# Kernel optimization log

Measured on AMD Instinct MI355X. Metric: run time of the kernel, lower is better.

## Reference

```python
import jax, jax.numpy as jnp
import numpy as np

HID = 16  # comparator hidden channels, Conv1(2,16) -> Conv1(16,1)


def setup_inputs() -> dict:
    key = jax.random.key(0)
    k0, k1, k2 = jax.random.split(key, 3)
    B, N = 32, 512
    x = jax.random.normal(k0, (B, 1, N), dtype=jnp.float32)
    # xavier_uniform for 1x1 convs, zero bias (as in PermNet.__init__)
    g1 = (6.0 / (2 + HID)) ** 0.5
    g2 = (6.0 / (HID + 1)) ** 0.5
    w1 = jax.random.uniform(k1, (HID, 2), jnp.float32, -g1, g1)
    b1 = jnp.zeros((HID,), jnp.float32)
    w2 = jax.random.uniform(k2, (1, HID), jnp.float32, -g2, g2)
    b2 = jnp.zeros((1,), jnp.float32)
    lr = jnp.ones((1,), jnp.float32)  # learned step size, used via abs()
    return {"x": x, "w1": w1, "b1": b1, "w2": w2, "b2": b2, "lr": lr,
            "steps": 8, "temp": 1}


def reference(x, w1, b1, w2, b2, lr, steps, temp):
    B, C, N = x.shape  # C == 1 (scalar set elements)
    temp = jnp.asarray(temp, x.dtype)

    # --- Comparator: pairwise 1x1-conv MLP over all (i, j) pairs ---
    xi = jnp.broadcast_to(x[:, 0, :, None], (B, N, N))  # element i
    xj = jnp.broadcast_to(x[:, 0, None, :], (B, N, N))  # element j
    pairs = jnp.stack([xi, xj], axis=1)                  # (B, 2, N, N)
    h = jax.nn.relu(jnp.einsum('oc,bcij->boij', w1, pairs)
                    + b1[None, :, None, None])           # (B, HID, N, N)
    c = (jnp.einsum('oc,bcij->boij', w2, h)
         + b2[None, :, None, None])[:, 0]                # (B, N, N)
    c = c - jnp.swapaxes(c, -1, -2)  # antisymmetric ordering cost C(i,j)=-C(j,i)

    # --- calculate_assignment: iterative differentiable permutation ---
    # a[b, i, k] = weight of element i being placed at position k
    lr_abs = jnp.abs(lr)[0]
    a0 = jnp.full((B, N, N), 1.0 / N, dtype=x.dtype)

    def step(a, _):
        csum = jnp.cumsum(a, axis=-1)      # sum_{l<=k} a[., j, l]
        total = csum[..., -1:]
        left = csum - a                     # sum_{l<k}
        right = total - csum                # sum_{l>k}
        m = right - left                    # (B, N, N)
        # d(total cost)/d a_{ik} = sum_j C_{ij} * (right_{jk} - left_{jk})
        grad = jnp.einsum('bij,bjk->bik', c, m)
        a_new = jax.nn.softmax((a - lr_abs * grad) / temp, axis=-1)
        return a_new, None

    a, _ = jax.lax.scan(step, a0, None, length=steps)

    # --- apply_assignment: permute elements into positions ---
    y = jnp.einsum('bci,bik->bck', x, a)  # (B, 1, N)
    return y, a
```

## Files before the change

### kernel.cpp

```cpp
#include <hip/hip_runtime.h>
#include <hip/hip_bf16.h>
#include <math.h>

#define B_   32
#define N_   512
#define HID_ 16

typedef __attribute__((ext_vector_type(8))) short bf16x8;
typedef __attribute__((ext_vector_type(4))) float f32x4;

union U8 { ushort u[8]; uint4 v; };
union U4 { ushort u[4]; uint2 v; };

__device__ __forceinline__ ushort f2bf(float f) {
    __hip_bfloat16 h = __float2bfloat16(f);
    return *reinterpret_cast<ushort*>(&h);
}
__device__ __forceinline__ float bf2f(ushort u) {
    return __uint_as_float(((unsigned int)u) << 16);
}

__device__ __forceinline__ void gload16(const void* g, void* l) {
    __builtin_amdgcn_global_load_lds(
        (const __attribute__((address_space(1))) unsigned int*)g,
        (__attribute__((address_space(3))) unsigned int*)l,
        16, 0, 0);
}

__device__ __forceinline__ int pidx(int r, int c) {
    return r * N_ + ((c + ((r >> 3) << 2)) & (N_ - 1));
}

__global__ __launch_bounds__(256)
void init_kernel(const float* __restrict__ x,
                 const float* __restrict__ w1,
                 const float* __restrict__ b1,
                 const float* __restrict__ w2,
                 ushort* __restrict__ cB,
                 float* __restrict__ v)
{
    __shared__ float sw1[2*HID_], sb1[HID_], sw2[HID_];
    __shared__ float red[4];
    int tid = threadIdx.x;
    if (tid < 2*HID_) sw1[tid] = w1[tid];
    if (tid < HID_)   { sb1[tid] = b1[tid]; sw2[tid] = w2[tid]; }
    __syncthreads();

    int rowg = blockIdx.x * 2 + (tid >> 7);
    int b    = rowg >> 9;
    int col  = (tid & 127) * 4;
    float xi = x[rowg];
    float4 xj = *(const float4*)&x[b*N_ + col];
    float xjv[4] = {xj.x, xj.y, xj.z, xj.w};

    float s1[4] = {}, s2[4] = {};
#pragma unroll
    for (int o = 0; o < HID_; ++o) {
        float wa = sw1[2*o], wb = sw1[2*o+1], bo = sb1[o], wo = sw2[o];
        float Ao = fmaf(wa, xi, bo);
        float Co = fmaf(wb, xi, bo);
#pragma unroll
        for (int e = 0; e < 4; ++e) {
            s1[e] = fmaf(wo, fmaxf(fmaf(wb, xjv[e], Ao), 0.f), s1[e]);
            s2[e] = fmaf(wo, fmaxf(fmaf(wa, xjv[e], Co), 0.f), s2[e]);
        }
    }

    float rs = 0.f;
    U4 cb;
#pragma unroll
    for (int e = 0; e < 4; ++e) {
        float cv = s1[e] - s2[e];
        rs += cv;
        cb.u[e] = f2bf(cv);
    }
    *(uint2*)&cB[(size_t)rowg * N_ + col] = cb.v;

#pragma unroll
    for (int off = 1; off < 64; off <<= 1) rs += __shfl_xor(rs, off);
    int w = tid >> 6;
    if ((tid & 63) == 0) red[w] = rs;
    __syncthreads();
    if (tid < 2) v[blockIdx.x * 2 + tid] = red[2*tid] + red[2*tid + 1];
}

__global__ __launch_bounds__(512)
void fused_kernel(const ushort* __restrict__ cB,
                  const ushort* __restrict__ aTin,
                  const ushort* __restrict__ aBin,
                  ushort* __restrict__ aTout,
                  ushort* __restrict__ aBout,
                  float* __restrict__ aout,
                  const float* __restrict__ v,
                  const float* __restrict__ lr,
                  const int* __restrict__ temp,
                  int first, int last)
{
    __shared__ char smem[131072];
    ushort* As = (ushort*)smem;
    ushort* Bs = (ushort*)(smem + 8192);
    float*  Pl = (float*)smem;

    int iblk = blockIdx.x;
    int r8 = iblk & 7, m = iblk >> 3;
    int b  = r8 + ((m >> 3) << 3);
    int i0 = (m & 7) * 64;

    const size_t MATOFF = (size_t)b * N_ * N_;
    int tid = threadIdx.x, lane = tid & 63, w = tid >> 6;

    if (!first) {
        const ushort* Ag = cB   + MATOFF + (size_t)i0 * N_;
        const ushort* Bg = aTin + MATOFF;
        f32x4 acc[4][4] = {};

        for (int kt = 0; kt < N_/64; ++kt) {
            int j0 = kt * 64;
            {
                int r = tid >> 3, s = tid & 7;
                gload16(Ag + (size_t)r * N_ + j0 + ((s ^ (r & 7)) << 3),
                        (char*)As + w*1024 + lane*16);
            }
#pragma unroll
            for (int c = 0; c < 8; ++c) {
                int r = c*8 + (lane >> 3), s = lane & 7;
                gload16(Bg + (size_t)(w*64 + r) * N_ + j0 + ((s ^ (r & 7)) << 3),
                        (char*)Bs + w*8192 + c*1024 + lane*16);
            }
            __syncthreads();

#pragma unroll
            for (int kk = 0; kk < 2; ++kk) {
                bf16x8 af[4], bb[4];
#pragma unroll
                for (int f = 0; f < 4; ++f) {
                    int ra = f*16 + (lane & 15);
                    int sa = kk*4 + (lane >> 4);
                    af[f] = *(const bf16x8*)((char*)As + ra*128 + ((sa ^ (ra & 7)) << 4));
                    bb[f] = *(const bf16x8*)((char*)Bs + w*8192 + ra*128 + ((sa ^ (ra & 7)) << 4));
                }
#pragma unroll
                for (int i = 0; i < 4; ++i)
#pragma unroll
                    for (int j = 0; j < 4; ++j)
                        acc[i][j] = __builtin_amdgcn_mfma_f32_16x16x32_bf16(
                                        af[i], bb[j], acc[i][j], 0, 0, 0);
            }
            __syncthreads();
        }

        {
            int h = lane >> 4, cl = lane & 15;
#pragma unroll
            for (int i = 0; i < 4; ++i)
#pragma unroll
                for (int j = 0; j < 4; ++j)
#pragma unroll
                    for (int r = 0; r < 4; ++r)
                        Pl[pidx(i*16 + h*4 + r, w*64 + j*16 + cl)] = acc[i][j][r];
        }
        __syncthreads();
    }

    float lrv = fabsf(lr[0]);
    float ti  = 1.0f / (float)temp[0];

    for (int q = 0; q < 8; ++q) {
        int row  = w*8 + q;
        int grow = i0 + row;
        float vr = v[b*N_ + grow];

        float pv[8], av[8];
        if (first) {
#pragma unroll
            for (int e = 0; e < 8; ++e) { pv[e] = vr * (1.0f/N_); av[e] = 1.0f/N_; }
        } else {
            int rot = (row >> 3) << 2;
            int c0  = (lane*8     + rot) & (N_-1);
            int c1  = (lane*8 + 4 + rot) & (N_-1);
            f32x4 p0 = *(const f32x4*)&Pl[row*N_ + c0];
            f32x4 p1 = *(const f32x4*)&Pl[row*N_ + c1];
            pv[0]=p0[0]; pv[1]=p0[1]; pv[2]=p0[2]; pv[3]=p0[3];
            pv[4]=p1[0]; pv[5]=p1[1]; pv[6]=p1[2]; pv[7]=p1[3];
            U8 ab;
            ab.v = *(const uint4*)&aBin[MATOFF + (size_t)grow * N_ + lane*8];
#pragma unroll
            for (int e = 0; e < 8; ++e) av[e] = bf2f(ab.u[e]);
        }

        float cs[8], run = 0.f;
#pragma unroll
        for (int e = 0; e < 8; ++e) { run += pv[e]; cs[e] = run; }
        float laneTot = run;
        float sc = laneTot;
#pragma unroll
        for (int off = 1; off < 64; off <<= 1) {
            float t = __shfl_up(sc, off);
            if (lane >= off) sc += t;
        }
        float excl = sc - laneTot;

        float l[8];
#pragma unroll
        for (int e = 0; e < 8; ++e) {
            float Q    = excl + cs[e];
            float grad = vr - 2.f*Q + pv[e];
            l[e] = (av[e] - lrv*grad) * ti;
        }

        float mx = l[0];
#pragma unroll
        for (int e = 1; e < 8; ++e) mx = fmaxf(mx, l[e]);
#pragma unroll
        for (int off = 1; off < 64; off <<= 1) mx = fmaxf(mx, __shfl_xor(mx, off));

        float ex[8], s = 0.f;
#pragma unroll
        for (int e = 0; e < 8; ++e) { ex[e] = __expf(l[e] - mx); s += ex[e]; }
#pragma unroll
        for (int off = 1; off < 64; off <<= 1) s += __shfl_xor(s, off);

        float inv = 1.0f / s;
#pragma unroll
        for (int e = 0; e < 8; ++e) ex[e] *= inv;

        size_t gbase = MATOFF + (size_t)grow * N_ + lane*8;
        if (last) {
            *(float4*)&aout[gbase]     = make_float4(ex[0], ex[1], ex[2], ex[3]);
            *(float4*)&aout[gbase + 4] = make_float4(ex[4], ex[5], ex[6], ex[7]);
        } else {
            U8 ob;
#pragma unroll
            for (int e = 0; e < 8; ++e) ob.u[e] = f2bf(ex[e]);
            *(uint4*)&aBout[gbase] = ob.v;
            int rot = (row >> 3) << 2;
            int c0  = (lane*8     + rot) & (N_-1);
            int c1  = (lane*8 + 4 + rot) & (N_-1);
            *(f32x4*)&Pl[row*N_ + c0] = f32x4{ex[0], ex[1], ex[2], ex[3]};
            *(f32x4*)&Pl[row*N_ + c1] = f32x4{ex[4], ex[5], ex[6], ex[7]};
        }
    }

    if (!last) {
        __syncthreads();
#pragma unroll
        for (int p = 0; p < 8; ++p) {
            int k   = p*64 + (tid >> 3);
            int ii0 = (tid & 7) * 8;
            U8 ob;
#pragma unroll
            for (int e = 0; e < 8; ++e) ob.u[e] = f2bf(Pl[pidx(ii0 + e, k)]);
            *(uint4*)&aTout[MATOFF + (size_t)k * N_ + i0 + ii0] = ob.v;
        }
    }
}

__global__ __launch_bounds__(256)
void y_kernel(const float* __restrict__ x,
              const float* __restrict__ a,
              float* __restrict__ y)
{
    __shared__ float xs[N_];
    __shared__ float red[4][64];
    int b  = blockIdx.y;
    int k0 = blockIdx.x * 64;
    int tid = threadIdx.x;
    xs[tid]       = x[b*N_ + tid];
    xs[tid + 256] = x[b*N_ + tid + 256];
    __syncthreads();

    int kl = tid & 63, strip = tid >> 6;
    const float* A = a + (size_t)b * N_ * N_;
    float acc = 0.f;
    int i0 = strip * 128;
#pragma unroll 4
    for (int i = i0; i < i0 + 128; ++i)
        acc = fmaf(xs[i], A[(size_t)i * N_ + k0 + kl], acc);
    red[strip][kl] = acc;
    __syncthreads();
    if (strip == 0)
        y[b*N_ + k0 + kl] = red[0][kl] + red[1][kl] + red[2][kl] + red[3][kl];
}

extern "C" void kernel_launch(void* const* d_in, const int* in_sizes, int n_in,
                              void* d_out, int out_size, void* d_ws, size_t ws_size,
                              hipStream_t stream)
{
    const float* x  = (const float*)d_in[0];
    const float* w1 = (const float*)d_in[1];
    const float* b1 = (const float*)d_in[2];
    const float* w2 = (const float*)d_in[3];
    const float* lr   = (const float*)d_in[5];
    const int*   temp = (const int*)d_in[7];

    float* y = (float*)d_out;
    float* a = y + B_ * N_;

    const size_t MAT = (size_t)B_ * N_ * N_;
    ushort* cB  = (ushort*)d_ws;
    ushort* aT0 = cB  + MAT;
    ushort* aT1 = aT0 + MAT;
    ushort* aB0 = aT1 + MAT;
    ushort* aB1 = aB0 + MAT;
    float*  v   = (float*)(aB1 + MAT);

    hipLaunchKernelGGL(init_kernel, dim3(B_*N_/2), dim3(256), 0, stream,
                       x, w1, b1, w2, cB, v);

    hipLaunchKernelGGL(fused_kernel, dim3(256), dim3(512), 0, stream,
                       cB, aT1, aB1, aT0, aB0, a, v, lr, temp, 1, 0);
    int cur = 0;
    for (int s = 1; s < 7; ++s) {
        ushort* tin  = cur ? aT1 : aT0;
        ushort* binp = cur ? aB1 : aB0;
        ushort* tout = cur ? aT0 : aT1;
        ushort* bout = cur ? aB0 : aB1;
        hipLaunchKernelGGL(fused_kernel, dim3(256), dim3(512), 0, stream,
                           cB, tin, binp, tout, bout, a, v, lr, temp, 0, 0);
        cur ^= 1;
    }
    {
        ushort* tin  = cur ? aT1 : aT0;
        ushort* binp = cur ? aB1 : aB0;
        hipLaunchKernelGGL(fused_kernel, dim3(256), dim3(512), 0, stream,
                           cB, tin, binp, aT0, aB0, a, v, lr, temp, 0, 1);
    }
    hipLaunchKernelGGL(y_kernel, dim3(8, B_), dim3(256), 0, stream, x, a, y);
}
```

Before: 252.4 us.

## Fuse all steps into one persistent cooperative kernel with grid syncs

Replaces the init kernel, eight per-step launches and the y kernel with a single cooperative kernel. Steps are separated by grid.sync, each block keeps its row-major assignment slice in registers, and y is accumulated in-kernel through partial sums. This removes launch gaps, the row-major bf16 copy round-trip through global memory, and the separate y pass that re-read the full output matrix. The cost is grid-wide barrier overhead, a requirement that all 256 blocks be co-resident, and higher register pressure from the per-row state kept across steps.

Result: slower. 855.0 us (+238.7%).

```diff
diff --git a/kernel.cpp b/kernel.cpp
--- a/kernel.cpp
+++ b/kernel.cpp
@@ -1,6 +1,9 @@
 #include <hip/hip_runtime.h>
+#include <hip/hip_cooperative_groups.h>
 #include <hip/hip_bf16.h>
 #include <math.h>
+
+namespace cg = cooperative_groups;
 
 #define B_   32
 #define N_   512
@@ -10,7 +13,6 @@
 typedef __attribute__((ext_vector_type(4))) float f32x4;
 
 union U8 { ushort u[8]; uint4 v; };
-union U4 { ushort u[4]; uint2 v; };
 
 __device__ __forceinline__ ushort f2bf(float f) {
     __hip_bfloat16 h = __float2bfloat16(f);
@@ -31,255 +33,255 @@
     return r * N_ + ((c + ((r >> 3) << 2)) & (N_ - 1));
 }
 
-__global__ __launch_bounds__(256)
-void init_kernel(const float* __restrict__ x,
+__global__ __launch_bounds__(512, 1)
+void perm_kernel(const float* __restrict__ x,
                  const float* __restrict__ w1,
                  const float* __restrict__ b1,
                  const float* __restrict__ w2,
+                 const float* __restrict__ lr,
+                 const int* __restrict__ temp,
                  ushort* __restrict__ cB,
-                 float* __restrict__ v)
+                 ushort* __restrict__ aT0,
+                 ushort* __restrict__ aT1,
+                 float* __restrict__ ypart,
+                 float* __restrict__ dout)
 {
-    __shared__ float sw1[2*HID_], sb1[HID_], sw2[HID_];
-    __shared__ float red[4];
-    int tid = threadIdx.x;
-    if (tid < 2*HID_) sw1[tid] = w1[tid];
-    if (tid < HID_)   { sb1[tid] = b1[tid]; sw2[tid] = w2[tid]; }
-    __syncthreads();
-
-    int rowg = blockIdx.x * 2 + (tid >> 7);
-    int b    = rowg >> 9;
-    int col  = (tid & 127) * 4;
-    float xi = x[rowg];
-    float4 xj = *(const float4*)&x[b*N_ + col];
-    float xjv[4] = {xj.x, xj.y, xj.z, xj.w};
-
-    float s1[4] = {}, s2[4] = {};
-#pragma unroll
-    for (int o = 0; o < HID_; ++o) {
-        float wa = sw1[2*o], wb = sw1[2*o+1], bo = sb1[o], wo = sw2[o];
-        float Ao = fmaf(wa, xi, bo);
-        float Co = fmaf(wb, xi, bo);
-#pragma unroll
-        for (int e = 0; e < 4; ++e) {
-            s1[e] = fmaf(wo, fmaxf(fmaf(wb, xjv[e], Ao), 0.f), s1[e]);
-            s2[e] = fmaf(wo, fmaxf(fmaf(wa, xjv[e], Co), 0.f), s2[e]);
-        }
-    }
-
-    float rs = 0.f;
-    U4 cb;
-#pragma unroll
-    for (int e = 0; e < 4; ++e) {
-        float cv = s1[e] - s2[e];
-        rs += cv;
-        cb.u[e] = f2bf(cv);
-    }
-    *(uint2*)&cB[(size_t)rowg * N_ + col] = cb.v;
-
-#pragma unroll
-    for (int off = 1; off < 64; off <<= 1) rs += __shfl_xor(rs, off);
-    int w = tid >> 6;
-    if ((tid & 63) == 0) red[w] = rs;
-    __syncthreads();
-    if (tid < 2) v[blockIdx.x * 2 + tid] = red[2*tid] + red[2*tid + 1];
-}
-
-__global__ __launch_bounds__(512)
-void fused_kernel(const ushort* __restrict__ cB,
-                  const ushort* __restrict__ aTin,
-                  const ushort* __restrict__ aBin,
-                  ushort* __restrict__ aTout,
-                  ushort* __restrict__ aBout,
-                  float* __restrict__ aout,
-                  const float* __restrict__ v,
-                  const float* __restrict__ lr,
-                  const int* __restrict__ temp,
-                  int first, int last)
-{
+    cg::grid_group grid = cg::this_grid();
+
     __shared__ char smem[131072];
+    __shared__ float sw1[2*HID_], sb1v[HID_], sw2v[HID_], v_s[64];
     ushort* As = (ushort*)smem;
     ushort* Bs = (ushort*)(smem + 8192);
     float*  Pl = (float*)smem;
+    float*  yred = (float*)smem;
+
+    int tid = threadIdx.x, lane = tid & 63, w = tid >> 6;
+
+    if (tid < 2*HID_) sw1[tid] = w1[tid];
+    if (tid < HID_)   { sb1v[tid] = b1[tid]; sw2v[tid] = w2[tid]; }
+    __syncthreads();
 
     int iblk = blockIdx.x;
     int r8 = iblk & 7, m = iblk >> 3;
     int b  = r8 + ((m >> 3) << 3);
     int i0 = (m & 7) * 64;
-
     const size_t MATOFF = (size_t)b * N_ * N_;
-    int tid = threadIdx.x, lane = tid & 63, w = tid >> 6;
-
-    if (!first) {
-        const ushort* Ag = cB   + MATOFF + (size_t)i0 * N_;
-        const ushort* Bg = aTin + MATOFF;
-        f32x4 acc[4][4] = {};
-
-        for (int kt = 0; kt < N_/64; ++kt) {
-            int j0 = kt * 64;
+
+    float lrv = fabsf(lr[0]);
+    float ti  = 1.0f / (float)temp[0];
+
+    {
+        int k0 = lane * 8;
+        float4 xj0 = *(const float4*)&x[b*N_ + k0];
+        float4 xj1 = *(const float4*)&x[b*N_ + k0 + 4];
+        float xjv[8] = {xj0.x, xj0.y, xj0.z, xj0.w, xj1.x, xj1.y, xj1.z, xj1.w};
+        for (int q = 0; q < 8; ++q) {
+            int grow = i0 + w*8 + q;
+            float xi = x[b*N_ + grow];
+            float s1[8] = {}, s2[8] = {};
+            for (int o = 0; o < HID_; ++o) {
+                float wa = sw1[2*o], wb = sw1[2*o+1], bo = sb1v[o], wo = sw2v[o];
+                float Ao = fmaf(wa, xi, bo);
+                float Co = fmaf(wb, xi, bo);
+#pragma unroll
+                for (int e = 0; e < 8; ++e) {
+                    s1[e] = fmaf(wo, fmaxf(fmaf(wb, xjv[e], Ao), 0.f), s1[e]);
+                    s2[e] = fmaf(wo, fmaxf(fmaf(wa, xjv[e], Co), 0.f), s2[e]);
+                }
+            }
+            float rs = 0.f;
+            U8 cb;
+#pragma unroll
+            for (int e = 0; e < 8; ++e) {
+                float cv = s1[e] - s2[e];
+                rs += cv;
+                cb.u[e] = f2bf(cv);
+            }
+            *(uint4*)&cB[MATOFF + (size_t)grow * N_ + k0] = cb.v;
+#pragma unroll
+            for (int off = 1; off < 64; off <<= 1) rs += __shfl_xor(rs, off);
+            if (lane == 0) v_s[w*8 + q] = rs;
+        }
+    }
+    __threadfence();
+    __syncthreads();
+
+    bf16x8 avq[8];
+    float  ysum[8] = {};
+
+    for (int s = 0; s < 8; ++s) {
+        if (s > 0) {
+            __threadfence();
+            grid.sync();
+
+            const ushort* Ag = cB + MATOFF + (size_t)i0 * N_;
+            const ushort* Bg = ((s & 1) ? aT0 : aT1) + MATOFF;
+            f32x4 acc[4][4] = {};
+
+            for (int kt = 0; kt < N_/64; ++kt) {
+                int j0 = kt * 64;
+                {
+                    int r = tid >> 3, sl = tid & 7;
+                    gload16(Ag + (size_t)r * N_ + j0 + ((sl ^ (r & 7)) << 3),
+                            (char*)As + w*1024 + lane*16);
+                }
+#pragma unroll
+                for (int c = 0; c < 8; ++c) {
+                    int r = c*8 + (lane >> 3), sl = lane & 7;
+                    gload16(Bg + (size_t)(w*64 + r) * N_ + j0 + ((sl ^ (r & 7)) << 3),
+                            (char*)Bs + w*8192 + c*1024 + lane*16);
+                }
+                __syncthreads();
+
+#pragma unroll
+                for (int kk = 0; kk < 2; ++kk) {
+                    bf16x8 af[4], bb[4];
+#pragma unroll
+                    for (int f = 0; f < 4; ++f) {
+                        int ra = f*16 + (lane & 15);
+                        int sa = kk*4 + (lane >> 4);
+                        af[f] = *(const bf16x8*)((char*)As + ra*128 + ((sa ^ (ra & 7)) << 4));
+                        bb[f] = *(const bf16x8*)((char*)Bs + w*8192 + ra*128 + ((sa ^ (ra & 7)) << 4));
+                    }
+#pragma unroll
+                    for (int i = 0; i < 4; ++i)
+#pragma unroll
+                        for (int j = 0; j < 4; ++j)
+                            acc[i][j] = __builtin_amdgcn_mfma_f32_16x16x32_bf16(
+                                            af[i], bb[j], acc[i][j], 0, 0, 0);
+                }
+                __syncthreads();
+            }
+
             {
-                int r = tid >> 3, s = tid & 7;
-                gload16(Ag + (size_t)r * N_ + j0 + ((s ^ (r & 7)) << 3),
-                        (char*)As + w*1024 + lane*16);
-            }
-#pragma unroll
-            for (int c = 0; c < 8; ++c) {
-                int r = c*8 + (lane >> 3), s = lane & 7;
-                gload16(Bg + (size_t)(w*64 + r) * N_ + j0 + ((s ^ (r & 7)) << 3),
-                        (char*)Bs + w*8192 + c*1024 + lane*16);
-            }
-            __syncthreads();
-
-#pragma unroll
-            for (int kk = 0; kk < 2; ++kk) {
-                bf16x8 af[4], bb[4];
-#pragma unroll
-                for (int f = 0; f < 4; ++f) {
-                    int ra = f*16 + (lane & 15);
-                    int sa = kk*4 + (lane >> 4);
-                    af[f] = *(const bf16x8*)((char*)As + ra*128 + ((sa ^ (ra & 7)) << 4));
-                    bb[f] = *(const bf16x8*)((char*)Bs + w*8192 + ra*128 + ((sa ^ (ra & 7)) << 4));
-                }
+                int h = lane >> 4, cl = lane & 15;
 #pragma unroll
                 for (int i = 0; i < 4; ++i)
 #pragma unroll
                     for (int j = 0; j < 4; ++j)
-                        acc[i][j] = __builtin_amdgcn_mfma_f32_16x16x32_bf16(
-                                        af[i], bb[j], acc[i][j], 0, 0, 0);
+#pragma unroll
+                        for (int r = 0; r < 4; ++r)
+                            Pl[pidx(i*16 + h*4 + r, w*64 + j*16 + cl)] = acc[i][j][r];
             }
             __syncthreads();
         }
 
-        {
-            int h = lane >> 4, cl = lane & 15;
-#pragma unroll
-            for (int i = 0; i < 4; ++i)
-#pragma unroll
-                for (int j = 0; j < 4; ++j)
-#pragma unroll
-                    for (int r = 0; r < 4; ++r)
-                        Pl[pidx(i*16 + h*4 + r, w*64 + j*16 + cl)] = acc[i][j][r];
+#pragma unroll
+        for (int q = 0; q < 8; ++q) {
+            int row  = w*8 + q;
+            int grow = i0 + row;
+            float vr = v_s[row];
+
+            float pv[8], av[8];
+            if (s == 0) {
+#pragma unroll
+                for (int e = 0; e < 8; ++e) { pv[e] = vr * (1.0f/N_); av[e] = 1.0f/N_; }
+            } else {
+                int rot = (row >> 3) << 2;
+                int c0  = (lane*8     + rot) & (N_-1);
+                int c1  = (lane*8 + 4 + rot) & (N_-1);
+                f32x4 p0 = *(const f32x4*)&Pl[row*N_ + c0];
+                f32x4 p1 = *(const f32x4*)&Pl[row*N_ + c1];
+                pv[0]=p0[0]; pv[1]=p0[1]; pv[2]=p0[2]; pv[3]=p0[3];
+                pv[4]=p1[0]; pv[5]=p1[1]; pv[6]=p1[2]; pv[7]=p1[3];
+#pragma unroll
+                for (int e = 0; e < 8; ++e) av[e] = bf2f(((ushort)avq[q][e]));
+            }
+
+            float cs[8], run = 0.f;
+#pragma unroll
+            for (int e = 0; e < 8; ++e) { run += pv[e]; cs[e] = run; }
+            float laneTot = run;
+            float sc = laneTot;
+#pragma unroll
+            for (int off = 1; off < 64; off <<= 1) {
+                float t = __shfl_up(sc, off);
+                if (lane >= off) sc += t;
+            }
+            float excl = sc - laneTot;
+
+            float l[8];
+#pragma unroll
+            for (int e = 0; e < 8; ++e) {
+                float Q    = excl + cs[e];
+                float grad = vr - 2.f*Q + pv[e];
+                l[e] = (av[e] - lrv*grad) * ti;
+            }
+
+            float mx = l[0];
+#pragma unroll
+            for (int e = 1; e < 8; ++e) mx = fmaxf(mx, l[e]);
+#pragma unroll
+            for (int off = 1; off < 64; off <<= 1) mx = fmaxf(mx, __shfl_xor(mx, off));
+
+            float ex[8], ssum = 0.f;
+#pragma unroll
+            for (int e = 0; e < 8; ++e) { ex[e] = __expf(l[e] - mx); ssum += ex[e]; }
+#pragma unroll
+            for (int off = 1; off < 64; off <<= 1) ssum += __shfl_xor(ssum, off);
+
+            float inv = 1.0f / ssum;
+#pragma unroll
+            for (int e = 0; e < 8; ++e) ex[e] *= inv;
+
+            if (s < 7) {
+                bf16x8 nb;
+#pragma unroll
+                for (int e = 0; e < 8; ++e) nb[e] = (short)f2bf(ex[e]);
+                avq[q] = nb;
+                int rot = (row >> 3) << 2;
+                int c0  = (lane*8     + rot) & (N_-1);
+                int c1  = (lane*8 + 4 + rot) & (N_-1);
+                *(f32x4*)&Pl[row*N_ + c0] = f32x4{ex[0], ex[1], ex[2], ex[3]};
+                *(f32x4*)&Pl[row*N_ + c1] = f32x4{ex[4], ex[5], ex[6], ex[7]};
+            } else {
+                size_t gbase = MATOFF + (size_t)grow * N_ + lane*8;
+                float* aout = dout + B_ * N_;
+                *(float4*)&aout[gbase]     = make_float4(ex[0], ex[1], ex[2], ex[3]);
+                *(float4*)&aout[gbase + 4] = make_float4(ex[4], ex[5], ex[6], ex[7]);
+                float xr = x[b*N_ + grow];
+#pragma unroll
+                for (int e = 0; e < 8; ++e) ysum[e] = fmaf(xr, ex[e], ysum[e]);
+            }
         }
-        __syncthreads();
-    }
-
-    float lrv = fabsf(lr[0]);
-    float ti  = 1.0f / (float)temp[0];
-
-    for (int q = 0; q < 8; ++q) {
-        int row  = w*8 + q;
-        int grow = i0 + row;
-        float vr = v[b*N_ + grow];
-
-        float pv[8], av[8];
-        if (first) {
-#pragma unroll
-            for (int e = 0; e < 8; ++e) { pv[e] = vr * (1.0f/N_); av[e] = 1.0f/N_; }
-        } else {
-            int rot = (row >> 3) << 2;
-            int c0  = (lane*8     + rot) & (N_-1);
-            int c1  = (lane*8 + 4 + rot) & (N_-1);
-            f32x4 p0 = *(const f32x4*)&Pl[row*N_ + c0];
-            f32x4 p1 = *(const f32x4*)&Pl[row*N_ + c1];
-            pv[0]=p0[0]; pv[1]=p0[1]; pv[2]=p0[2]; pv[3]=p0[3];
-            pv[4]=p1[0]; pv[5]=p1[1]; pv[6]=p1[2]; pv[7]=p1[3];
-            U8 ab;
-            ab.v = *(const uint4*)&aBin[MATOFF + (size_t)grow * N_ + lane*8];
-#pragma unroll
-            for (int e = 0; e < 8; ++e) av[e] = bf2f(ab.u[e]);
-        }
-
-        float cs[8], run = 0.f;
-#pragma unroll
-        for (int e = 0; e < 8; ++e) { run += pv[e]; cs[e] = run; }
-        float laneTot = run;
-        float sc = laneTot;
-#pragma unroll
-        for (int off = 1; off < 64; off <<= 1) {
-            float t = __shfl_up(sc, off);
-            if (lane >= off) sc += t;
-        }
-        float excl = sc - laneTot;
-
-        float l[8];
-#pragma unroll
-        for (int e = 0; e < 8; ++e) {
-            float Q    = excl + cs[e];
-            float grad = vr - 2.f*Q + pv[e];
-            l[e] = (av[e] - lrv*grad) * ti;
-        }
-
-        float mx = l[0];
-#pragma unroll
-        for (int e = 1; e < 8; ++e) mx = fmaxf(mx, l[e]);
-#pragma unroll
-        for (int off = 1; off < 64; off <<= 1) mx = fmaxf(mx, __shfl_xor(mx, off));
-
-        float ex[8], s = 0.f;
-#pragma unroll
-        for (int e = 0; e < 8; ++e) { ex[e] = __expf(l[e] - mx); s += ex[e]; }
-#pragma unroll
-        for (int off = 1; off < 64; off <<= 1) s += __shfl_xor(s, off);
-
-        float inv = 1.0f / s;
-#pragma unroll
-        for (int e = 0; e < 8; ++e) ex[e] *= inv;
-
-        size_t gbase = MATOFF + (size_t)grow * N_ + lane*8;
-        if (last) {
-            *(float4*)&aout[gbase]     = make_float4(ex[0], ex[1], ex[2], ex[3]);
-            *(float4*)&aout[gbase + 4] = make_float4(ex[4], ex[5], ex[6], ex[7]);
-        } else {
-            U8 ob;
-#pragma unroll
-            for (int e = 0; e < 8; ++e) ob.u[e] = f2bf(ex[e]);
-            *(uint4*)&aBout[gbase] = ob.v;
-            int rot = (row >> 3) << 2;
-            int c0  = (lane*8     + rot) & (N_-1);
-            int c1  = (lane*8 + 4 + rot) & (N_-1);
-            *(f32x4*)&Pl[row*N_ + c0] = f32x4{ex[0], ex[1], ex[2], ex[3]};
-            *(f32x4*)&Pl[row*N_ + c1] = f32x4{ex[4], ex[5], ex[6], ex[7]};
+
+        if (s < 7) {
+            __syncthreads();
+            ushort* aTout = (s & 1) ? aT1 : aT0;
+#pragma unroll
+            for (int p = 0; p < 8; ++p) {
+                int k   = p*64 + (tid >> 3);
+                int ii0 = (tid & 7) * 8;
+                U8 ob;
+#pragma unroll
+                for (int e = 0; e < 8; ++e) ob.u[e] = f2bf(Pl[pidx(ii0 + e, k)]);
+                *(uint4*)&aTout[MATOFF + (size_t)k * N_ + i0 + ii0] = ob.v;
+            }
+            __syncthreads();
         }
     }
 
-    if (!last) {
-        __syncthreads();
-#pragma unroll
-        for (int p = 0; p < 8; ++p) {
-            int k   = p*64 + (tid >> 3);
-            int ii0 = (tid & 7) * 8;
-            U8 ob;
-#pragma unroll
-            for (int e = 0; e < 8; ++e) ob.u[e] = f2bf(Pl[pidx(ii0 + e, k)]);
-            *(uint4*)&aTout[MATOFF + (size_t)k * N_ + i0 + ii0] = ob.v;
-        }
+    __syncthreads();
+    *(f32x4*)&yred[w*512 + lane*8]     = f32x4{ysum[0], ysum[1], ysum[2], ysum[3]};
+    *(f32x4*)&yred[w*512 + lane*8 + 4] = f32x4{ysum[4], ysum[5], ysum[6], ysum[7]};
+    __syncthreads();
+    {
+        float acc = 0.f;
+#pragma unroll
+        for (int wv = 0; wv < 8; ++wv) acc += yred[wv*512 + tid];
+        ypart[(size_t)(b*8 + (i0 >> 6)) * 512 + tid] = acc;
     }
-}
-
-__global__ __launch_bounds__(256)
-void y_kernel(const float* __restrict__ x,
-              const float* __restrict__ a,
-              float* __restrict__ y)
-{
-    __shared__ float xs[N_];
-    __shared__ float red[4][64];
-    int b  = blockIdx.y;
-    int k0 = blockIdx.x * 64;
-    int tid = threadIdx.x;
-    xs[tid]       = x[b*N_ + tid];
-    xs[tid + 256] = x[b*N_ + tid + 256];
-    __syncthreads();
-
-    int kl = tid & 63, strip = tid >> 6;
-    const float* A = a + (size_t)b * N_ * N_;
-    float acc = 0.f;
-    int i0 = strip * 128;
-#pragma unroll 4
-    for (int i = i0; i < i0 + 128; ++i)
-        acc = fmaf(xs[i], A[(size_t)i * N_ + k0 + kl], acc);
-    red[strip][kl] = acc;
-    __syncthreads();
-    if (strip == 0)
-        y[b*N_ + k0 + kl] = red[0][kl] + red[1][kl] + red[2][kl] + red[3][kl];
+
+    __threadfence();
+    grid.sync();
+
+    if (i0 == 0) {
+        float acc = 0.f;
+#pragma unroll
+        for (int t8 = 0; t8 < 8; ++t8)
+            acc += ypart[(size_t)(b*8 + t8) * 512 + tid];
+        dout[b*N_ + tid] = acc;
+    }
 }
 
 extern "C" void kernel_launch(void* const* d_in, const int* in_sizes, int n_in,
@@ -293,37 +295,18 @@
     const float* lr   = (const float*)d_in[5];
     const int*   temp = (const int*)d_in[7];
 
-    float* y = (float*)d_out;
-    float* a = y + B_ * N_;
+    float* dout = (float*)d_out;
 
     const size_t MAT = (size_t)B_ * N_ * N_;
-    ushort* cB  = (ushort*)d_ws;
-    ushort* aT0 = cB  + MAT;
-    ushort* aT1 = aT0 + MAT;
-    ushort* aB0 = aT1 + MAT;
-    ushort* aB1 = aB0 + MAT;
-    float*  v   = (float*)(aB1 + MAT);
-
-    hipLaunchKernelGGL(init_kernel, dim3(B_*N_/2), dim3(256), 0, stream,
-                       x, w1, b1, w2, cB, v);
-
-    hipLaunchKernelGGL(fused_kernel, dim3(256), dim3(512), 0, stream,
-                       cB, aT1, aB1, aT0, aB0, a, v, lr, temp, 1, 0);
-    int cur = 0;
-    for (int s = 1; s < 7; ++s) {
-        ushort* tin  = cur ? aT1 : aT0;
-        ushort* binp = cur ? aB1 : aB0;
-        ushort* tout = cur ? aT0 : aT1;
-        ushort* bout = cur ? aB0 : aB1;
-        hipLaunchKernelGGL(fused_kernel, dim3(256), dim3(512), 0, stream,
-                           cB, tin, binp, tout, bout, a, v, lr, temp, 0, 0);
-        cur ^= 1;
-    }
-    {
-        ushort* tin  = cur ? aT1 : aT0;
-        ushort* binp = cur ? aB1 : aB0;
-        hipLaunchKernelGGL(fused_kernel, dim3(256), dim3(512), 0, stream,
-                           cB, tin, binp, aT0, aB0, a, v, lr, temp, 0, 1);
-    }
-    hipLaunchKernelGGL(y_kernel, dim3(8, B_), dim3(256), 0, stream, x, a, y);
-}
+    ushort* cB    = (ushort*)d_ws;
+    ushort* aT0   = cB  + MAT;
+    ushort* aT1   = aT0 + MAT;
+    float*  ypart = (float*)(aT1 + MAT);
+
+    void* args[] = { (void*)&x, (void*)&w1, (void*)&b1, (void*)&w2,
+                     (void*)&lr, (void*)&temp,
+                     (void*)&cB, (void*)&aT0, (void*)&aT1,
+                     (void*)&ypart, (void*)&dout };
+    hipLaunchCooperativeKernel((const void*)perm_kernel,
+                               dim3(256), dim3(512), args, 0, stream);
+}
```
